# Optimization experiments

Hardware: AMD Instinct MI355X
Metric: run time of the kernel (lower is better)

Reference implementation:

```python
import jax, jax.numpy as jnp
import numpy as np

B, N, E = 4, 10000, 170000
F_IN, F, H = 256, 128, 4
LEAKY_SLOPE = 0.2  # TF default alpha for tf.nn.leaky_relu


def setup_inputs() -> dict:
    key = jax.random.key(0)
    ks = jax.random.split(key, 6)
    x = jax.random.normal(ks[0], (B, N, F_IN), jnp.float32)
    src = jnp.sort(jax.random.randint(ks[1], (E,), 0, N, jnp.int32))
    dst = jax.random.randint(ks[2], (E,), 0, N, jnp.int32)
    W_mlp = jax.random.normal(ks[3], (H, F_IN, F), jnp.float32) / np.float32(np.sqrt(F_IN))
    b_mlp = jnp.zeros((H, F), jnp.float32)
    W_attn = jax.random.normal(ks[4], (H, 2 * F, 1), jnp.float32) / np.float32(np.sqrt(2 * F))
    return {"x": x, "W_mlp": W_mlp, "b_mlp": b_mlp, "W_attn": W_attn, "src": src, "dst": dst}


def reference(x, W_mlp, b_mlp, W_attn, src, dst):
    n_edges = src.shape[0]
    batch = x.shape[0]
    # per-head node transform: [B,H,N,F]
    h = jnp.einsum('bnf,hfe->bhne', x, W_mlp) + b_mlp[None, :, None, :]
    # split attention kernel: score = leaky_relu([h_src||h_dst] @ W_attn)
    a_src = W_attn[:, :F, 0]  # [H,F]
    a_dst = W_attn[:, F:, 0]  # [H,F]
    # faithful quirk: the original normalizes and scatters attention from the
    # LAST batch element only (attention_scores[-1]) and applies it to all batches
    hl = h[-1]  # [H,N,F]
    p_src = jnp.einsum('hnf,hf->hn', hl, a_src)
    p_dst = jnp.einsum('hnf,hf->hn', hl, a_dst)
    s = p_src[:, src] + p_dst[:, dst]                 # [H,E]
    e = jnp.exp(jnp.clip(jax.nn.leaky_relu(s, LEAKY_SLOPE), -2.0, 2.0))
    denom = jax.ops.segment_sum(e.T, src, num_segments=N).T  # [H,N]
    norm = e / denom[:, src]                          # [H,E]
    outs = []
    for hi in range(H):  # small fixed head loop (limits peak memory)
        g = jnp.take(h[:, hi], dst, axis=1) * norm[hi][None, :, None]  # [B,E,F]
        g = jnp.swapaxes(g, 0, 1).reshape(n_edges, batch * F)          # [E,B*F]
        agg = jax.ops.segment_sum(g, src, num_segments=N)              # [N,B*F]
        outs.append(agg.reshape(N, batch, F).transpose(1, 0, 2))       # [B,N,F]
    return jnp.concatenate(outs, axis=-1)  # [B,N,H*F]
```

## Files before the change

### kernel.cpp

```cpp
#include <hip/hip_runtime.h>
#include <hip/hip_bf16.h>

constexpr int Bq  = 4;
constexpr int Nn  = 10000;
constexpr int Eq  = 170000;
constexpr int FIN = 256;
constexpr int Ff  = 128;
constexpr int Hh  = 4;
constexpr int C   = Hh * Ff;
constexpr float LEAKY = 0.2f;

typedef short short4v __attribute__((ext_vector_type(4)));
typedef short short8  __attribute__((ext_vector_type(8)));
typedef float f32x4   __attribute__((ext_vector_type(4)));

static __device__ __forceinline__ unsigned short f2bf(float f) {
    unsigned int u = __float_as_uint(f);
    u = u + 0x7fffu + ((u >> 16) & 1u);
    return (unsigned short)(u >> 16);
}
static __device__ __forceinline__ float bf2f(unsigned short b) {
    return __uint_as_float(((unsigned int)b) << 16);
}

__global__ __launch_bounds__(256) void prep_kernel(
    const float* __restrict__ W, const float* __restrict__ Wattn,
    const float* __restrict__ bmlp, const int* __restrict__ src,
    unsigned short* __restrict__ Wf, float* __restrict__ wa,
    float* __restrict__ bsd, int* __restrict__ row_start)
{
    int bid = blockIdx.x, t = threadIdx.x;
    if (bid < 512) {
        int cc = bid;
        int k = t;
        float v = W[(size_t)(cc >> 7) * FIN * Ff + (size_t)k * Ff + (cc & 127)];
        int w = cc >> 7, j = (cc >> 4) & 7, ln = cc & 15;
        int ks = k >> 5, quad = (k >> 3) & 3, el = k & 7;
        size_t u = ((size_t)((w * 8 + j) * 8 + ks) * 4 + quad) * 16 + ln;
        Wf[u * 8 + el] = f2bf(v);
    } else if (bid == 512) {
        int hi = t >> 6, kb = t & 63;
        #pragma unroll
        for (int i = 0; i < 4; ++i) {
            int k = kb + i * 64;
            float ss = 0.f, sd = 0.f;
            const float* wrow = W + ((size_t)hi * FIN + k) * Ff;
            const float* as = Wattn + hi * 2 * Ff;
            const float* ad = as + Ff;
            for (int f = 0; f < Ff; f += 4) {
                float4 wv = *(const float4*)(wrow + f);
                float4 av = *(const float4*)(as + f);
                float4 dv = *(const float4*)(ad + f);
                ss += wv.x * av.x + wv.y * av.y + wv.z * av.z + wv.w * av.w;
                sd += wv.x * dv.x + wv.y * dv.y + wv.z * dv.z + wv.w * dv.w;
            }
            wa[(0 * 4 + hi) * FIN + k] = ss;
            wa[(1 * 4 + hi) * FIN + k] = sd;
        }
        if (t < 8) {
            int v = t & 1, hh = t >> 1;
            float s = 0.f;
            for (int f = 0; f < Ff; ++f)
                s += bmlp[hh * Ff + f] * Wattn[hh * 2 * Ff + v * Ff + f];
            bsd[v * 4 + hh] = s;
        }
    } else {
        int n = (bid - 513) * 256 + t;
        if (n > Nn) return;
        int lo = 0, hi = Eq;
        while (lo < hi) { int mid = (lo + hi) >> 1; if (src[mid] < n) lo = mid + 1; else hi = mid; }
        row_start[n] = lo;
    }
}

__global__ __launch_bounds__(256) void xprep_proj_kernel(
    const float* __restrict__ X, const float* __restrict__ wa,
    const float* __restrict__ bsd, unsigned short* __restrict__ Xb,
    float* __restrict__ psT, float* __restrict__ pdT)
{
    int n0 = blockIdx.x * 8;
    int t  = threadIdx.x;
    int r  = t >> 5;
    int c  = t & 31;
    int k8 = c * 8;
    float s[8];
    #pragma unroll
    for (int i = 0; i < 8; ++i) s[i] = 0.f;

    #pragma unroll
    for (int b = 0; b < Bq; ++b) {
        const float* p = X + ((size_t)b * Nn + n0 + r) * FIN + k8;
        float4 v0 = *(const float4*)p, v1 = *(const float4*)(p + 4);
        short8 v;
        v[0] = (short)f2bf(v0.x); v[1] = (short)f2bf(v0.y);
        v[2] = (short)f2bf(v0.z); v[3] = (short)f2bf(v0.w);
        v[4] = (short)f2bf(v1.x); v[5] = (short)f2bf(v1.y);
        v[6] = (short)f2bf(v1.z); v[7] = (short)f2bf(v1.w);
        *(short8*)(Xb + ((size_t)(n0 + r) * Bq + b) * FIN + k8) = v;
        if (b == Bq - 1) {
            #pragma unroll
            for (int i = 0; i < 8; ++i) {
                const float* w = wa + (size_t)i * FIN + k8;
                float4 w0 = *(const float4*)w, w1 = *(const float4*)(w + 4);
                s[i] = v0.x * w0.x + v0.y * w0.y + v0.z * w0.z + v0.w * w0.w
                     + v1.x * w1.x + v1.y * w1.y + v1.z * w1.z + v1.w * w1.w;
            }
        }
    }
    #pragma unroll
    for (int off = 1; off < 32; off <<= 1)
        #pragma unroll
        for (int i = 0; i < 8; ++i) s[i] += __shfl_xor(s[i], off, 64);
    if (c == 0) {
        int n = n0 + r;
        #pragma unroll
        for (int hi = 0; hi < 4; ++hi) {
            psT[n * 4 + hi] = s[hi]     + bsd[hi];
            pdT[n * 4 + hi] = s[4 + hi] + bsd[4 + hi];
        }
    }
}

__global__ __launch_bounds__(256) void edge_denom_kernel(
    const int* __restrict__ dst, const int* __restrict__ row_start,
    const float* __restrict__ psT, const float* __restrict__ pdT,
    float* __restrict__ eed, float* __restrict__ denom)
{
    int wv = threadIdx.x >> 6, t = threadIdx.x & 63;
    int n = blockIdx.x * 4 + wv;
    int e0 = row_start[n], e1 = row_start[n + 1];
    float4 ps = *(const float4*)(psT + (size_t)n * 4);
    float4 acc = {0.f, 0.f, 0.f, 0.f};
    for (int e = e0 + t; e < e1; e += 64) {
        int d = dst[e];
        float4 pd = *(const float4*)(pdT + (size_t)d * 4);
        float4 ev;
        { float sc = ps.x + pd.x; float lr = sc > 0.f ? sc : LEAKY * sc;
          ev.x = __expf(fminf(fmaxf(lr, -2.f), 2.f)); }
        { float sc = ps.y + pd.y; float lr = sc > 0.f ? sc : LEAKY * sc;
          ev.y = __expf(fminf(fmaxf(lr, -2.f), 2.f)); }
        { float sc = ps.z + pd.z; float lr = sc > 0.f ? sc : LEAKY * sc;
          ev.z = __expf(fminf(fmaxf(lr, -2.f), 2.f)); }
        { float sc = ps.w + pd.w; float lr = sc > 0.f ? sc : LEAKY * sc;
          ev.w = __expf(fminf(fmaxf(lr, -2.f), 2.f)); }
        *(float4*)(eed + (size_t)e * 4) = ev;
        acc.x += ev.x; acc.y += ev.y; acc.z += ev.z; acc.w += ev.w;
    }
    #pragma unroll
    for (int off = 1; off < 64; off <<= 1) {
        acc.x += __shfl_xor(acc.x, off, 64);
        acc.y += __shfl_xor(acc.y, off, 64);
        acc.z += __shfl_xor(acc.z, off, 64);
        acc.w += __shfl_xor(acc.w, off, 64);
    }
    if (t == 0) *(float4*)(denom + (size_t)n * 4) = acc;
}

__global__ __launch_bounds__(256, 5) void gather_gemm_kernel(
    const unsigned short* __restrict__ Xb, const float* __restrict__ eed,
    const int* __restrict__ row_start, const int* __restrict__ dst,
    const unsigned short* __restrict__ Wf, const float* __restrict__ bias,
    const float* __restrict__ denom, float* __restrict__ out)
{
    __shared__ unsigned short As[Hh * 16 * 256];

    const int n0  = blockIdx.x * 4;
    const int t   = threadIdx.x;
    const int b   = t >> 6;
    const int off = t * 4;
    const int k0  = (t & 63) * 4;

    const float4* eed4 = (const float4*)eed;

    for (int nl = 0; nl < 4; ++nl) {
        const int n  = n0 + nl;
        const int e0 = row_start[n], e1 = row_start[n + 1];

        float acc[4][4];
        #pragma unroll
        for (int hi = 0; hi < 4; ++hi)
            #pragma unroll
            for (int j = 0; j < 4; ++j) acc[hi][j] = 0.f;

        int e = e0;
        for (; e + 4 <= e1; e += 4) {
            int d0 = dst[e], d1 = dst[e + 1], d2 = dst[e + 2], d3 = dst[e + 3];
            short4v v0 = *(const short4v*)(Xb + (size_t)d0 * 1024 + off);
            short4v v1 = *(const short4v*)(Xb + (size_t)d1 * 1024 + off);
            short4v v2 = *(const short4v*)(Xb + (size_t)d2 * 1024 + off);
            short4v v3 = *(const short4v*)(Xb + (size_t)d3 * 1024 + off);
            float4 ev0 = eed4[e], ev1 = eed4[e + 1], ev2 = eed4[e + 2], ev3 = eed4[e + 3];
            float w[4][4] = {
                {ev0.x, ev0.y, ev0.z, ev0.w},
                {ev1.x, ev1.y, ev1.z, ev1.w},
                {ev2.x, ev2.y, ev2.z, ev2.w},
                {ev3.x, ev3.y, ev3.z, ev3.w}};
            #pragma unroll
            for (int j = 0; j < 4; ++j) {
                float f0 = bf2f((unsigned short)v0[j]);
                float f1 = bf2f((unsigned short)v1[j]);
                float f2 = bf2f((unsigned short)v2[j]);
                float f3 = bf2f((unsigned short)v3[j]);
                #pragma unroll
                for (int hi = 0; hi < 4; ++hi)
                    acc[hi][j] += f0 * w[0][hi] + f1 * w[1][hi] + f2 * w[2][hi] + f3 * w[3][hi];
            }
        }
        for (; e < e1; ++e) {
            int d0 = dst[e];
            short4v v0 = *(const short4v*)(Xb + (size_t)d0 * 1024 + off);
            float4 ev0 = eed4[e];
            #pragma unroll
            for (int j = 0; j < 4; ++j) {
                float f = bf2f((unsigned short)v0[j]);
                acc[0][j] += f * ev0.x; acc[1][j] += f * ev0.y;
                acc[2][j] += f * ev0.z; acc[3][j] += f * ev0.w;
            }
        }

        float4 dn = *(const float4*)(denom + (size_t)n * 4);
        float inv[4];
        inv[0] = dn.x != 0.f ? 1.f / dn.x : 0.f;
        inv[1] = dn.y != 0.f ? 1.f / dn.y : 0.f;
        inv[2] = dn.z != 0.f ? 1.f / dn.z : 0.f;
        inv[3] = dn.w != 0.f ? 1.f / dn.w : 0.f;

        const int row = nl * 4 + b;
        const int swz = (row & 7) << 3;
        #pragma unroll
        for (int hi = 0; hi < 4; ++hi) {
            short4v o;
            #pragma unroll
            for (int j = 0; j < 4; ++j) o[j] = (short)f2bf(acc[hi][j] * inv[hi]);
            *(short4v*)&As[(hi * 4096 + row * 256 + k0) ^ swz] = o;
        }
    }
    __syncthreads();

    const int lane = t & 63;
    const int hi   = t >> 6;
    const int quad = lane >> 4, ln = lane & 15;
    const int rswz = (ln & 7) << 3;

    f32x4 macc[8];
    #pragma unroll
    for (int j = 0; j < 8; ++j) macc[j] = (f32x4){0.f, 0.f, 0.f, 0.f};

    const short8* Wf8 = (const short8*)Wf;
    #pragma unroll
    for (int ks = 0; ks < 8; ++ks) {
        short8 a = *(const short8*)&As[(hi * 4096 + ln * 256 + ks * 32 + quad * 8) ^ rswz];
        #pragma unroll
        for (int j = 0; j < 8; ++j) {
            short8 bf = Wf8[(size_t)((hi * 8 + j) * 8 + ks) * 64 + lane];
            macc[j] = __builtin_amdgcn_mfma_f32_16x16x32_bf16(a, bf, macc[j], 0, 0, 0);
        }
    }

    const int nn = n0 + quad;
    const float flag = denom[(size_t)nn * 4 + hi] != 0.f ? 1.f : 0.f;
    #pragma unroll
    for (int j = 0; j < 8; ++j) {
        int colf = j * 16 + ln;
        float bv = bias[hi * Ff + colf] * flag;
        #pragma unroll
        for (int r = 0; r < 4; ++r) {
            out[((size_t)r * Nn + nn) * C + hi * Ff + colf] = macc[j][r] + bv;
        }
    }
}

extern "C" void kernel_launch(void* const* d_in, const int* in_sizes, int n_in,
                              void* d_out, int out_size, void* d_ws, size_t ws_size,
                              hipStream_t stream)
{
    const float* x      = (const float*)d_in[0];
    const float* W_mlp  = (const float*)d_in[1];
    const float* b_mlp  = (const float*)d_in[2];
    const float* W_attn = (const float*)d_in[3];
    const int*   src    = (const int*)d_in[4];
    const int*   dst    = (const int*)d_in[5];
    float* out = (float*)d_out;

    unsigned short* Xb  = (unsigned short*)d_ws;
    unsigned short* Wf  = Xb + (size_t)Nn * Bq * FIN;
    float* eed   = (float*)(Wf + (size_t)C * FIN);
    float* psT   = eed + (size_t)Eq * 4;
    float* pdT   = psT + (size_t)Nn * 4;
    float* denom = pdT + (size_t)Nn * 4;
    float* wa    = denom + (size_t)Nn * 4;
    float* bsd   = wa + 2 * 4 * FIN;
    int*   row_st = (int*)(bsd + 16);

    hipLaunchKernelGGL(prep_kernel, dim3(553), dim3(256), 0, stream,
                       W_mlp, W_attn, b_mlp, src, Wf, wa, bsd, row_st);
    hipLaunchKernelGGL(xprep_proj_kernel, dim3(Nn / 8), dim3(256), 0, stream,
                       x, wa, bsd, Xb, psT, pdT);
    hipLaunchKernelGGL(edge_denom_kernel, dim3(Nn / 4), dim3(256), 0, stream,
                       dst, row_st, psT, pdT, eed, denom);
    hipLaunchKernelGGL(gather_gemm_kernel, dim3(Nn / 4), dim3(256), 0, stream,
                       Xb, eed, row_st, dst, Wf, b_mlp, denom, out);
}
```

Measured before the change: 230.0 us.

## Bucket edges by destination tile so gather blocks sweep Xb tile by tile

The edge kernel now counting-sorts each node's edges into 10 buckets by dst>>10 using wave ballots, and writes reordered dst and edge weights plus per-node bucket offsets. The gather kernel loops over tiles in the outer loop and over its 4 nodes in the inner loop, keeping 64 accumulators live. All concurrent blocks then touch the same ~1024-row slice of Xb at roughly the same time, which is meant to improve L2 reuse of the gathered features. The cost is extra ballot work and writes in the edge kernel, higher register pressure (occupancy hint lowered from 5 to 4), and a smaller unroll in the gather loop.

```diff
diff --git a/kernel.cpp b/kernel.cpp
--- a/kernel.cpp
+++ b/kernel.cpp
@@ -9,6 +9,10 @@
 constexpr int Hh  = 4;
 constexpr int C   = Hh * Ff;
 constexpr float LEAKY = 0.2f;
+
+constexpr int TILE_SHIFT = 10;
+constexpr int NT  = 10;
+constexpr int NT1 = NT + 1;
 
 typedef short short4v __attribute__((ext_vector_type(4)));
 typedef short short8  __attribute__((ext_vector_type(8)));
@@ -121,18 +125,50 @@
     }
 }
 
-__global__ __launch_bounds__(256) void edge_denom_kernel(
+__global__ __launch_bounds__(256) void edge_sort_denom_kernel(
     const int* __restrict__ dst, const int* __restrict__ row_start,
     const float* __restrict__ psT, const float* __restrict__ pdT,
-    float* __restrict__ eed, float* __restrict__ denom)
-{
-    int wv = threadIdx.x >> 6, t = threadIdx.x & 63;
-    int n = blockIdx.x * 4 + wv;
-    int e0 = row_start[n], e1 = row_start[n + 1];
+    int* __restrict__ dstR, float* __restrict__ eedR,
+    int* __restrict__ rts, float* __restrict__ denom)
+{
+    const int wv = threadIdx.x >> 6, lane = threadIdx.x & 63;
+    const int n = blockIdx.x * 4 + wv;
+    const int e0 = row_start[n], e1 = row_start[n + 1];
+    const int deg = e1 - e0;
+    const int nch = (deg + 63) >> 6;
+    const unsigned long long below = (1ull << lane) - 1ull;
+
+    int tot[NT];
+    #pragma unroll
+    for (int t2 = 0; t2 < NT; ++t2) tot[t2] = 0;
+    for (int c = 0; c < nch; ++c) {
+        int e = e0 + c * 64 + lane;
+        bool valid = e < e1;
+        int d = dst[valid ? e : e0];
+        int tl = d >> TILE_SHIFT;
+        #pragma unroll
+        for (int t2 = 0; t2 < NT; ++t2)
+            tot[t2] += (int)__popcll(__ballot(valid && tl == t2));
+    }
+    int base[NT];
+    {
+        int run = e0;
+        #pragma unroll
+        for (int t2 = 0; t2 < NT; ++t2) { base[t2] = run; run += tot[t2]; }
+    }
+    if (lane == 0) {
+        #pragma unroll
+        for (int t2 = 0; t2 < NT; ++t2) rts[(size_t)n * NT1 + t2] = base[t2];
+        rts[(size_t)n * NT1 + NT] = e1;
+    }
+
     float4 ps = *(const float4*)(psT + (size_t)n * 4);
     float4 acc = {0.f, 0.f, 0.f, 0.f};
-    for (int e = e0 + t; e < e1; e += 64) {
-        int d = dst[e];
+    for (int c = 0; c < nch; ++c) {
+        int e = e0 + c * 64 + lane;
+        bool valid = e < e1;
+        int d = dst[valid ? e : e0];
+        int tl = d >> TILE_SHIFT;
         float4 pd = *(const float4*)(pdT + (size_t)d * 4);
         float4 ev;
         { float sc = ps.x + pd.x; float lr = sc > 0.f ? sc : LEAKY * sc;
@@ -143,8 +179,20 @@
           ev.z = __expf(fminf(fmaxf(lr, -2.f), 2.f)); }
         { float sc = ps.w + pd.w; float lr = sc > 0.f ? sc : LEAKY * sc;
           ev.w = __expf(fminf(fmaxf(lr, -2.f), 2.f)); }
-        *(float4*)(eed + (size_t)e * 4) = ev;
-        acc.x += ev.x; acc.y += ev.y; acc.z += ev.z; acc.w += ev.w;
+        if (valid) {
+            acc.x += ev.x; acc.y += ev.y; acc.z += ev.z; acc.w += ev.w;
+        }
+        int pos = 0;
+        #pragma unroll
+        for (int t2 = 0; t2 < NT; ++t2) {
+            unsigned long long m = __ballot(valid && tl == t2);
+            if (valid && tl == t2) pos = base[t2] + (int)__popcll(m & below);
+            base[t2] += (int)__popcll(m);
+        }
+        if (valid) {
+            dstR[pos] = d;
+            *(float4*)(eedR + (size_t)pos * 4) = ev;
+        }
     }
     #pragma unroll
     for (int off = 1; off < 64; off <<= 1) {
@@ -153,12 +201,13 @@
         acc.z += __shfl_xor(acc.z, off, 64);
         acc.w += __shfl_xor(acc.w, off, 64);
     }
-    if (t == 0) *(float4*)(denom + (size_t)n * 4) = acc;
-}
-
-__global__ __launch_bounds__(256, 5) void gather_gemm_kernel(
-    const unsigned short* __restrict__ Xb, const float* __restrict__ eed,
-    const int* __restrict__ row_start, const int* __restrict__ dst,
+    if (lane == 0) *(float4*)(denom + (size_t)n * 4) = acc;
+}
+
+__global__ __launch_bounds__(256, 4) void gather_gemm_kernel(
+    const unsigned short* __restrict__ Xb, const float* __restrict__ eedR,
+    const int* __restrict__ row_start, const int* __restrict__ rts,
+    const int* __restrict__ dstR,
     const unsigned short* __restrict__ Wf, const float* __restrict__ bias,
     const float* __restrict__ denom, float* __restrict__ out)
 {
@@ -170,68 +219,67 @@
     const int off = t * 4;
     const int k0  = (t & 63) * 4;
 
-    const float4* eed4 = (const float4*)eed;
-
-    for (int nl = 0; nl < 4; ++nl) {
-        const int n  = n0 + nl;
-        const int e0 = row_start[n], e1 = row_start[n + 1];
-
-        float acc[4][4];
+    const float4* eed4 = (const float4*)eedR;
+
+    float acc[4][4][4];
+    #pragma unroll
+    for (int nl = 0; nl < 4; ++nl)
         #pragma unroll
         for (int hi = 0; hi < 4; ++hi)
             #pragma unroll
-            for (int j = 0; j < 4; ++j) acc[hi][j] = 0.f;
-
-        int e = e0;
-        for (; e + 4 <= e1; e += 4) {
-            int d0 = dst[e], d1 = dst[e + 1], d2 = dst[e + 2], d3 = dst[e + 3];
-            short4v v0 = *(const short4v*)(Xb + (size_t)d0 * 1024 + off);
-            short4v v1 = *(const short4v*)(Xb + (size_t)d1 * 1024 + off);
-            short4v v2 = *(const short4v*)(Xb + (size_t)d2 * 1024 + off);
-            short4v v3 = *(const short4v*)(Xb + (size_t)d3 * 1024 + off);
-            float4 ev0 = eed4[e], ev1 = eed4[e + 1], ev2 = eed4[e + 2], ev3 = eed4[e + 3];
-            float w[4][4] = {
-                {ev0.x, ev0.y, ev0.z, ev0.w},
-                {ev1.x, ev1.y, ev1.z, ev1.w},
-                {ev2.x, ev2.y, ev2.z, ev2.w},
-                {ev3.x, ev3.y, ev3.z, ev3.w}};
-            #pragma unroll
-            for (int j = 0; j < 4; ++j) {
-                float f0 = bf2f((unsigned short)v0[j]);
-                float f1 = bf2f((unsigned short)v1[j]);
-                float f2 = bf2f((unsigned short)v2[j]);
-                float f3 = bf2f((unsigned short)v3[j]);
+            for (int j = 0; j < 4; ++j) acc[nl][hi][j] = 0.f;
+
+    for (int tl = 0; tl < NT; ++tl) {
+        #pragma unroll
+        for (int nl = 0; nl < 4; ++nl) {
+            const int n = n0 + nl;
+            int e  = rts[(size_t)n * NT1 + tl];
+            int ee = rts[(size_t)n * NT1 + tl + 1];
+            for (; e + 2 <= ee; e += 2) {
+                int d0 = dstR[e], d1 = dstR[e + 1];
+                short4v v0 = *(const short4v*)(Xb + (size_t)d0 * 1024 + off);
+                short4v v1 = *(const short4v*)(Xb + (size_t)d1 * 1024 + off);
+                float4 ev0 = eed4[e], ev1 = eed4[e + 1];
                 #pragma unroll
-                for (int hi = 0; hi < 4; ++hi)
-                    acc[hi][j] += f0 * w[0][hi] + f1 * w[1][hi] + f2 * w[2][hi] + f3 * w[3][hi];
+                for (int j = 0; j < 4; ++j) {
+                    float f0 = bf2f((unsigned short)v0[j]);
+                    float f1 = bf2f((unsigned short)v1[j]);
+                    acc[nl][0][j] += f0 * ev0.x + f1 * ev1.x;
+                    acc[nl][1][j] += f0 * ev0.y + f1 * ev1.y;
+                    acc[nl][2][j] += f0 * ev0.z + f1 * ev1.z;
+                    acc[nl][3][j] += f0 * ev0.w + f1 * ev1.w;
+                }
             }
-        }
-        for (; e < e1; ++e) {
-            int d0 = dst[e];
-            short4v v0 = *(const short4v*)(Xb + (size_t)d0 * 1024 + off);
-            float4 ev0 = eed4[e];
-            #pragma unroll
-            for (int j = 0; j < 4; ++j) {
-                float f = bf2f((unsigned short)v0[j]);
-                acc[0][j] += f * ev0.x; acc[1][j] += f * ev0.y;
-                acc[2][j] += f * ev0.z; acc[3][j] += f * ev0.w;
+            if (e < ee) {
+                int d0 = dstR[e];
+                short4v v0 = *(const short4v*)(Xb + (size_t)d0 * 1024 + off);
+                float4 ev0 = eed4[e];
+                #pragma unroll
+                for (int j = 0; j < 4; ++j) {
+                    float f = bf2f((unsigned short)v0[j]);
+                    acc[nl][0][j] += f * ev0.x; acc[nl][1][j] += f * ev0.y;
+                    acc[nl][2][j] += f * ev0.z; acc[nl][3][j] += f * ev0.w;
+                }
             }
         }
-
+    }
+
+    #pragma unroll
+    for (int nl = 0; nl < 4; ++nl) {
+        const int n = n0 + nl;
         float4 dn = *(const float4*)(denom + (size_t)n * 4);
         float inv[4];
         inv[0] = dn.x != 0.f ? 1.f / dn.x : 0.f;
         inv[1] = dn.y != 0.f ? 1.f / dn.y : 0.f;
         inv[2] = dn.z != 0.f ? 1.f / dn.z : 0.f;
         inv[3] = dn.w != 0.f ? 1.f / dn.w : 0.f;
-
         const int row = nl * 4 + b;
         const int swz = (row & 7) << 3;
         #pragma unroll
         for (int hi = 0; hi < 4; ++hi) {
             short4v o;
             #pragma unroll
-            for (int j = 0; j < 4; ++j) o[j] = (short)f2bf(acc[hi][j] * inv[hi]);
+            for (int j = 0; j < 4; ++j) o[j] = (short)f2bf(acc[nl][hi][j] * inv[hi]);
             *(short4v*)&As[(hi * 4096 + row * 256 + k0) ^ swz] = o;
         }
     }
@@ -284,20 +332,22 @@
 
     unsigned short* Xb  = (unsigned short*)d_ws;
     unsigned short* Wf  = Xb + (size_t)Nn * Bq * FIN;
-    float* eed   = (float*)(Wf + (size_t)C * FIN);
-    float* psT   = eed + (size_t)Eq * 4;
+    float* eedR  = (float*)(Wf + (size_t)C * FIN);
+    float* psT   = eedR + (size_t)Eq * 4;
     float* pdT   = psT + (size_t)Nn * 4;
     float* denom = pdT + (size_t)Nn * 4;
     float* wa    = denom + (size_t)Nn * 4;
     float* bsd   = wa + 2 * 4 * FIN;
     int*   row_st = (int*)(bsd + 16);
+    int*   dstR   = row_st + (Nn + 2);
+    int*   rts    = dstR + Eq;
 
     hipLaunchKernelGGL(prep_kernel, dim3(553), dim3(256), 0, stream,
                        W_mlp, W_attn, b_mlp, src, Wf, wa, bsd, row_st);
     hipLaunchKernelGGL(xprep_proj_kernel, dim3(Nn / 8), dim3(256), 0, stream,
                        x, wa, bsd, Xb, psT, pdT);
-    hipLaunchKernelGGL(edge_denom_kernel, dim3(Nn / 4), dim3(256), 0, stream,
-                       dst, row_st, psT, pdT, eed, denom);
+    hipLaunchKernelGGL(edge_sort_denom_kernel, dim3(Nn / 4), dim3(256), 0, stream,
+                       dst, row_st, psT, pdT, dstR, eedR, rts, denom);
     hipLaunchKernelGGL(gather_gemm_kernel, dim3(Nn / 4), dim3(256), 0, stream,
-                       Xb, eed, row_st, dst, Wf, b_mlp, denom, out);
-}
+                       Xb, eedR, row_st, rts, dstR, Wf, b_mlp, denom, out);
+}
```

Measured after the change: 239.3 us. +4.0%, slower.

## Process two nodes per block in parallel with wider 16-byte gathers

Applied to the files above, without the earlier changes.

The gather kernel now handles two nodes per block, with one 128-thread group per node running concurrently, instead of four nodes processed one after another. Each thread loads 8 bf16 values per neighbour with a 16-byte load instead of 4. The grid doubles, shared memory halves and the occupancy hint rises to 6. The goal is more memory-level parallelism and less serial per-node latency in the gather. The cost is that the MFMA stage now wastes half of its rows (lanes reuse rows 0-7 and only quads 0-1 store), so the weight matrix is reloaded per block for half the useful output.

```diff
diff --git a/kernel.cpp b/kernel.cpp
--- a/kernel.cpp
+++ b/kernel.cpp
@@ -156,83 +156,80 @@
     if (t == 0) *(float4*)(denom + (size_t)n * 4) = acc;
 }
 
-__global__ __launch_bounds__(256, 5) void gather_gemm_kernel(
+__global__ __launch_bounds__(256, 6) void gather_gemm_kernel(
     const unsigned short* __restrict__ Xb, const float* __restrict__ eed,
     const int* __restrict__ row_start, const int* __restrict__ dst,
     const unsigned short* __restrict__ Wf, const float* __restrict__ bias,
     const float* __restrict__ denom, float* __restrict__ out)
 {
-    __shared__ unsigned short As[Hh * 16 * 256];
-
-    const int n0  = blockIdx.x * 4;
-    const int t   = threadIdx.x;
-    const int b   = t >> 6;
-    const int off = t * 4;
-    const int k0  = (t & 63) * 4;
+    __shared__ unsigned short As[Hh * 8 * 256];
+
+    const int n0   = blockIdx.x * 2;
+    const int t    = threadIdx.x;
+    const int g    = t >> 7;
+    const int slot = t & 127;
+    const int b    = slot >> 5;
+    const int k0   = (slot & 31) * 8;
+    const int off  = slot * 8;
+
+    const int n  = n0 + g;
+    const int e0 = row_start[n], e1 = row_start[n + 1];
+
+    float acc[4][8];
+    #pragma unroll
+    for (int hi = 0; hi < 4; ++hi)
+        #pragma unroll
+        for (int j = 0; j < 8; ++j) acc[hi][j] = 0.f;
 
     const float4* eed4 = (const float4*)eed;
 
-    for (int nl = 0; nl < 4; ++nl) {
-        const int n  = n0 + nl;
-        const int e0 = row_start[n], e1 = row_start[n + 1];
-
-        float acc[4][4];
-        #pragma unroll
-        for (int hi = 0; hi < 4; ++hi)
-            #pragma unroll
-            for (int j = 0; j < 4; ++j) acc[hi][j] = 0.f;
-
-        int e = e0;
-        for (; e + 4 <= e1; e += 4) {
-            int d0 = dst[e], d1 = dst[e + 1], d2 = dst[e + 2], d3 = dst[e + 3];
-            short4v v0 = *(const short4v*)(Xb + (size_t)d0 * 1024 + off);
-            short4v v1 = *(const short4v*)(Xb + (size_t)d1 * 1024 + off);
-            short4v v2 = *(const short4v*)(Xb + (size_t)d2 * 1024 + off);
-            short4v v3 = *(const short4v*)(Xb + (size_t)d3 * 1024 + off);
-            float4 ev0 = eed4[e], ev1 = eed4[e + 1], ev2 = eed4[e + 2], ev3 = eed4[e + 3];
-            float w[4][4] = {
-                {ev0.x, ev0.y, ev0.z, ev0.w},
-                {ev1.x, ev1.y, ev1.z, ev1.w},
-                {ev2.x, ev2.y, ev2.z, ev2.w},
-                {ev3.x, ev3.y, ev3.z, ev3.w}};
-            #pragma unroll
-            for (int j = 0; j < 4; ++j) {
-                float f0 = bf2f((unsigned short)v0[j]);
-                float f1 = bf2f((unsigned short)v1[j]);
-                float f2 = bf2f((unsigned short)v2[j]);
-                float f3 = bf2f((unsigned short)v3[j]);
-                #pragma unroll
-                for (int hi = 0; hi < 4; ++hi)
-                    acc[hi][j] += f0 * w[0][hi] + f1 * w[1][hi] + f2 * w[2][hi] + f3 * w[3][hi];
-            }
-        }
-        for (; e < e1; ++e) {
-            int d0 = dst[e];
-            short4v v0 = *(const short4v*)(Xb + (size_t)d0 * 1024 + off);
-            float4 ev0 = eed4[e];
-            #pragma unroll
-            for (int j = 0; j < 4; ++j) {
-                float f = bf2f((unsigned short)v0[j]);
-                acc[0][j] += f * ev0.x; acc[1][j] += f * ev0.y;
-                acc[2][j] += f * ev0.z; acc[3][j] += f * ev0.w;
-            }
-        }
-
+    int e = e0;
+    for (; e + 4 <= e1; e += 4) {
+        int d0 = dst[e], d1 = dst[e + 1], d2 = dst[e + 2], d3 = dst[e + 3];
+        short8 v0 = *(const short8*)(Xb + (size_t)d0 * 1024 + off);
+        short8 v1 = *(const short8*)(Xb + (size_t)d1 * 1024 + off);
+        short8 v2 = *(const short8*)(Xb + (size_t)d2 * 1024 + off);
+        short8 v3 = *(const short8*)(Xb + (size_t)d3 * 1024 + off);
+        float4 ev0 = eed4[e], ev1 = eed4[e + 1], ev2 = eed4[e + 2], ev3 = eed4[e + 3];
+        #pragma unroll
+        for (int j = 0; j < 8; ++j) {
+            float f0 = bf2f((unsigned short)v0[j]);
+            float f1 = bf2f((unsigned short)v1[j]);
+            float f2 = bf2f((unsigned short)v2[j]);
+            float f3 = bf2f((unsigned short)v3[j]);
+            acc[0][j] += f0 * ev0.x + f1 * ev1.x + f2 * ev2.x + f3 * ev3.x;
+            acc[1][j] += f0 * ev0.y + f1 * ev1.y + f2 * ev2.y + f3 * ev3.y;
+            acc[2][j] += f0 * ev0.z + f1 * ev1.z + f2 * ev2.z + f3 * ev3.z;
+            acc[3][j] += f0 * ev0.w + f1 * ev1.w + f2 * ev2.w + f3 * ev3.w;
+        }
+    }
+    for (; e < e1; ++e) {
+        int d0 = dst[e];
+        short8 v0 = *(const short8*)(Xb + (size_t)d0 * 1024 + off);
+        float4 ev0 = eed4[e];
+        #pragma unroll
+        for (int j = 0; j < 8; ++j) {
+            float f = bf2f((unsigned short)v0[j]);
+            acc[0][j] += f * ev0.x; acc[1][j] += f * ev0.y;
+            acc[2][j] += f * ev0.z; acc[3][j] += f * ev0.w;
+        }
+    }
+
+    {
         float4 dn = *(const float4*)(denom + (size_t)n * 4);
         float inv[4];
         inv[0] = dn.x != 0.f ? 1.f / dn.x : 0.f;
         inv[1] = dn.y != 0.f ? 1.f / dn.y : 0.f;
         inv[2] = dn.z != 0.f ? 1.f / dn.z : 0.f;
         inv[3] = dn.w != 0.f ? 1.f / dn.w : 0.f;
-
-        const int row = nl * 4 + b;
-        const int swz = (row & 7) << 3;
+        const int row = g * 4 + b;
+        const int swz = row << 3;
         #pragma unroll
         for (int hi = 0; hi < 4; ++hi) {
-            short4v o;
+            short8 o;
             #pragma unroll
-            for (int j = 0; j < 4; ++j) o[j] = (short)f2bf(acc[hi][j] * inv[hi]);
-            *(short4v*)&As[(hi * 4096 + row * 256 + k0) ^ swz] = o;
+            for (int j = 0; j < 8; ++j) o[j] = (short)f2bf(acc[hi][j] * inv[hi]);
+            *(short8*)&As[(hi * 2048 + row * 256 + k0) ^ swz] = o;
         }
     }
     __syncthreads();
@@ -240,7 +237,7 @@
     const int lane = t & 63;
     const int hi   = t >> 6;
     const int quad = lane >> 4, ln = lane & 15;
-    const int rswz = (ln & 7) << 3;
+    const int lnr  = ln & 7;
 
     f32x4 macc[8];
     #pragma unroll
@@ -249,7 +246,7 @@
     const short8* Wf8 = (const short8*)Wf;
     #pragma unroll
     for (int ks = 0; ks < 8; ++ks) {
-        short8 a = *(const short8*)&As[(hi * 4096 + ln * 256 + ks * 32 + quad * 8) ^ rswz];
+        short8 a = *(const short8*)&As[(hi * 2048 + lnr * 256 + ks * 32 + quad * 8) ^ (lnr << 3)];
         #pragma unroll
         for (int j = 0; j < 8; ++j) {
             short8 bf = Wf8[(size_t)((hi * 8 + j) * 8 + ks) * 64 + lane];
@@ -257,15 +254,17 @@
         }
     }
 
-    const int nn = n0 + quad;
-    const float flag = denom[(size_t)nn * 4 + hi] != 0.f ? 1.f : 0.f;
-    #pragma unroll
-    for (int j = 0; j < 8; ++j) {
-        int colf = j * 16 + ln;
-        float bv = bias[hi * Ff + colf] * flag;
-        #pragma unroll
-        for (int r = 0; r < 4; ++r) {
-            out[((size_t)r * Nn + nn) * C + hi * Ff + colf] = macc[j][r] + bv;
+    if (quad < 2) {
+        const int nn = n0 + quad;
+        const float flag = denom[(size_t)nn * 4 + hi] != 0.f ? 1.f : 0.f;
+        #pragma unroll
+        for (int j = 0; j < 8; ++j) {
+            int colf = j * 16 + ln;
+            float bv = bias[hi * Ff + colf] * flag;
+            #pragma unroll
+            for (int r = 0; r < 4; ++r) {
+                out[((size_t)r * Nn + nn) * C + hi * Ff + colf] = macc[j][r] + bv;
+            }
         }
     }
 }
@@ -298,6 +297,6 @@
                        x, wa, bsd, Xb, psT, pdT);
     hipLaunchKernelGGL(edge_denom_kernel, dim3(Nn / 4), dim3(256), 0, stream,
                        dst, row_st, psT, pdT, eed, denom);
-    hipLaunchKernelGGL(gather_gemm_kernel, dim3(Nn / 4), dim3(256), 0, stream,
+    hipLaunchKernelGGL(gather_gemm_kernel, dim3(Nn / 2), dim3(256), 0, stream,
                        Xb, eed, row_st, dst, Wf, b_mlp, denom, out);
 }
```

Measured after the change: 263.1 us. +14.4%, slower.
